# Kernel tuning notes

Hardware: AMD Instinct MI355X
Metric: run time of the kernel (lower is better)

The kernel has to match this reference:

```python
import jax, jax.numpy as jnp
from jax import lax
import numpy as np

B, CIN, COUT, WDIM, RES = 8, 512, 512, 512, 64


def setup_inputs() -> dict:
    key = jax.random.key(0)
    k0, k1, k2, k3 = jax.random.split(key, 4)
    x = jax.random.normal(k0, (B, CIN, RES, RES), dtype=jnp.float32)
    w = jax.random.normal(k1, (B, WDIM), dtype=jnp.float32)
    weight = jax.random.normal(k2, (COUT, CIN, 3, 3), dtype=jnp.float32)
    bias = jnp.zeros((COUT,), dtype=jnp.float32)
    affine_w = jax.random.normal(k3, (CIN, WDIM), dtype=jnp.float32) * 0.02
    affine_b = jnp.zeros((CIN,), dtype=jnp.float32)
    return {"x": x, "w": w, "weight": weight, "bias": bias,
            "affine_w": affine_w, "affine_b": affine_b}


def reference(x, w, weight, bias, affine_w, affine_b):
    # style: [B, Cin] = affine(w)
    style = w @ affine_w.T + affine_b
    b, cin, h, wd = x.shape
    cout = weight.shape[0]
    # per-sample modulated weight: [B, Cout, Cin, 3, 3]
    wmod = weight[None, :, :, :, :] * style[:, None, :, None, None]
    # grouped conv with groups = batch: lhs [1, B*Cin, H, W], rhs [B*Cout, Cin, 3, 3]
    lhs = x.reshape(1, b * cin, h, wd)
    rhs = wmod.reshape(b * cout, cin, 3, 3)
    y = lax.conv_general_dilated(
        lhs, rhs,
        window_strides=(1, 1),
        padding=[(1, 1), (1, 1)],
        dimension_numbers=("NCHW", "OIHW", "NCHW"),
        feature_group_count=b,
    )
    y = y.reshape(b, cout, h, wd)
    return y + bias[None, :, None, None]
```

## Files before the change

### kernel.cpp

```cpp
#include <hip/hip_runtime.h>
#include <cstdint>
#include <cstddef>

#define BATCH 8
#define CIN   512
#define COUT  512
#define RES   64
#define HW    4096
#define WDIM  512

typedef short bf16x8 __attribute__((ext_vector_type(8)));
typedef float f32x4  __attribute__((ext_vector_type(4)));
typedef unsigned short ushort8 __attribute__((ext_vector_type(8)));

typedef const __attribute__((address_space(1))) void* gas_ptr;
typedef __attribute__((address_space(3))) void*       las_ptr;

__device__ __forceinline__ unsigned short f2bf(float f) {
    unsigned int u = __float_as_uint(f);
    u += 0x7fffu + ((u >> 16) & 1u);
    return (unsigned short)(u >> 16);
}

__global__ __launch_bounds__(256) void prep_kernel(
    const float* __restrict__ w, const float* __restrict__ aw,
    const float* __restrict__ ab, float* __restrict__ style,
    unsigned short* __restrict__ zpage,
    const float* __restrict__ wt, unsigned short* __restrict__ wr)
{
    __shared__ float buf[4608];
    int bid = blockIdx.x;
    int t = threadIdx.x;
    if (bid < 1024) {
        if (bid == 0 && t < 128) zpage[t] = 0;
        int wv = t >> 6, lane = t & 63;
        int idx = bid * 4 + wv;
        int b = idx >> 9, ci = idx & 511;
        const float* wrow = w + b * WDIM;
        const float* arow = aw + (size_t)ci * WDIM;
        float s = 0.f;
#pragma unroll
        for (int i = 0; i < WDIM / 64; ++i) s += arow[lane + i * 64] * wrow[lane + i * 64];
#pragma unroll
        for (int off = 32; off; off >>= 1) s += __shfl_down(s, off);
        if (lane == 0) style[idx] = s + ab[ci];
    } else {
        int co = bid - 1024;
#pragma unroll
        for (int r = 0; r < 18; ++r) buf[r * 256 + t] = wt[(size_t)co * 4608 + r * 256 + t];
        __syncthreads();
#pragma unroll
        for (int r = 0; r < 18; ++r) {
            int idx = r * 256 + t;
            int tap = idx >> 9, ci = idx & 511;
            wr[(size_t)tap * (COUT * CIN) + co * CIN + ci] = f2bf(buf[ci * 9 + tap]);
        }
    }
}

__global__ __launch_bounds__(256) void modtrans_kernel(
    const float* __restrict__ x, const float* __restrict__ style,
    unsigned short* __restrict__ xs)
{
    __shared__ float tile[64][65];
    int t = threadIdx.x;
    int hw0 = blockIdx.x * 64, ci0 = blockIdx.y * 64, b = blockIdx.z;
    int sub = t >> 6, lane = t & 63;
#pragma unroll
    for (int r = 0; r < 16; ++r) {
        int ci = r * 4 + sub;
        float s = style[b * CIN + ci0 + ci];
        tile[ci][lane] = x[((size_t)(b * CIN + ci0 + ci)) * HW + hw0 + lane] * s;
    }
    __syncthreads();
    int ci8 = (t & 7) * 8;
#pragma unroll
    for (int r = 0; r < 2; ++r) {
        int hw = r * 32 + (t >> 3);
        ushort8 v;
#pragma unroll
        for (int j = 0; j < 8; ++j) v[j] = f2bf(tile[ci8 + j][hw]);
        *(ushort8*)&xs[((size_t)b * HW + hw0 + hw) * CIN + ci0 + ci8] = v;
    }
}

__global__ __launch_bounds__(256) void conv_kernel(
    const unsigned short* __restrict__ xs,
    const unsigned short* __restrict__ wr,
    const float* __restrict__ bias,
    const unsigned short* __restrict__ zpage,
    float* __restrict__ y)
{
    __shared__ __align__(16) unsigned short As[3 * 128 * 32];
    __shared__ __align__(16) unsigned short Bs[2 * 66 * 32];

    const int t   = threadIdx.x;
    const int bid = blockIdx.x;
    const int co0 = (bid >> 8) * 128;
    const int rem = bid & 255;
    const int h0  = (rem >> 3) * 2;
    const int b   = rem & 7;

    const int lane = t & 63;
    const int wv   = t >> 6;
    const int wm   = (wv & 1) * 64;
    const int wn   = (wv >> 1) * 64;
    const int r16  = lane & 15;
    const int quad = lane >> 4;

    if (t < 128) {
        int d = t >> 6, c = t & 63;
        int col = (c < 32) ? 0 : 65;
        Bs[(d * 66 + col) * 32 + (c & 31)] = 0;
    }

    f32x4 acc[4][4];
#pragma unroll
    for (int mi = 0; mi < 4; ++mi)
#pragma unroll
        for (int ni = 0; ni < 4; ++ni)
            acc[mi][ni] = (f32x4){0.f, 0.f, 0.f, 0.f};

    for (int kh = 0; kh < 3; ++kh) {
        const unsigned short* pA[6];
#pragma unroll
        for (int L = 0; L < 6; ++L) {
            int lin = L * 256 + t;
            int tap = kh * 3 + (lin >> 9);
            int q   = (lin >> 2) & 127;
            int c8  = ((lin & 3) ^ ((lin >> 3) & 3)) * 8;
            pA[L] = wr + (size_t)tap * (COUT * CIN) + (co0 + q) * CIN + c8;
        }
        const unsigned short* pB[2];
        int sB[2];
#pragma unroll
        for (int L = 0; L < 2; ++L) {
            int lin = L * 256 + t;
            int dh = lin >> 8, r8 = lin & 255;
            int wc = r8 >> 2;
            int rowp = dh * 66 + 1 + wc;
            int c8 = ((r8 & 3) ^ ((rowp >> 1) & 3)) * 8;
            int hp = h0 + dh + kh - 1;
            bool ok = (unsigned)hp < 64u;
            pB[L] = ok ? xs + ((size_t)b * HW + hp * 64 + wc) * CIN + c8 : zpage;
            sB[L] = ok ? 32 : 0;
        }

        for (int ch = 0; ch < 16; ++ch) {
#pragma unroll
            for (int L = 0; L < 6; ++L) {
                int lin = L * 256 + t;
                __builtin_amdgcn_global_load_lds((gas_ptr)pA[L], (las_ptr)&As[lin * 8], 16, 0, 0);
                pA[L] += 32;
            }
#pragma unroll
            for (int L = 0; L < 2; ++L) {
                int lin = L * 256 + t;
                int dh = lin >> 8, r8 = lin & 255;
                __builtin_amdgcn_global_load_lds((gas_ptr)pB[L],
                    (las_ptr)&Bs[(dh * 66 + 1) * 32 + r8 * 8], 16, 0, 0);
                pB[L] += sB[L];
            }
            __syncthreads();
#pragma unroll
            for (int kw = 0; kw < 3; ++kw) {
                bf16x8 af[4], bfv[4];
#pragma unroll
                for (int mi = 0; mi < 4; ++mi) {
                    int row = kw * 128 + wm + mi * 16 + r16;
                    int ck  = quad ^ ((row >> 1) & 3);
                    af[mi] = *(const bf16x8*)&As[row * 32 + ck * 8];
                }
#pragma unroll
                for (int ni = 0; ni < 4; ++ni) {
                    int n = wn + ni * 16 + r16;
                    int dh = n >> 6, wc = n & 63;
                    int row = dh * 66 + wc + kw;
                    int ck  = quad ^ ((row >> 1) & 3);
                    bfv[ni] = *(const bf16x8*)&Bs[row * 32 + ck * 8];
                }
#pragma unroll
                for (int mi = 0; mi < 4; ++mi)
#pragma unroll
                    for (int ni = 0; ni < 4; ++ni)
                        acc[mi][ni] = __builtin_amdgcn_mfma_f32_16x16x32_bf16(
                            af[mi], bfv[ni], acc[mi][ni], 0, 0, 0);
            }
            __syncthreads();
        }
    }

#pragma unroll
    for (int mi = 0; mi < 4; ++mi) {
#pragma unroll
        for (int r = 0; r < 4; ++r) {
            int m = co0 + wm + mi * 16 + quad * 4 + r;
            float bv = bias[m];
            size_t base = ((size_t)b * COUT + m) * HW + h0 * 64;
#pragma unroll
            for (int ni = 0; ni < 4; ++ni) {
                int n = wn + ni * 16 + r16;
                y[base + n] = acc[mi][ni][r] + bv;
            }
        }
    }
}

extern "C" void kernel_launch(void* const* d_in, const int* in_sizes, int n_in,
                              void* d_out, int out_size, void* d_ws, size_t ws_size,
                              hipStream_t stream)
{
    (void)in_sizes; (void)n_in; (void)out_size; (void)ws_size;
    const float* x    = (const float*)d_in[0];
    const float* w    = (const float*)d_in[1];
    const float* wt   = (const float*)d_in[2];
    const float* bias = (const float*)d_in[3];
    const float* aw   = (const float*)d_in[4];
    const float* ab   = (const float*)d_in[5];
    float* y = (float*)d_out;

    char* ws = (char*)d_ws;
    float*          style = (float*)ws;
    unsigned short* zpage = (unsigned short*)(ws + 16384);
    unsigned short* wr    = (unsigned short*)(ws + 32768);
    unsigned short* xs    = (unsigned short*)(ws + 4751360);

    prep_kernel<<<1536, 256, 0, stream>>>(w, aw, ab, style, zpage, wt, wr);
    modtrans_kernel<<<dim3(64, 8, 8), 256, 0, stream>>>(x, style, xs);
    conv_kernel<<<1024, 256, 0, stream>>>(xs, wr, bias, zpage, y);
}
```

Before: 268.7 us.

## Widen conv tile to four output rows with 512 threads and fuse prep kernels

The conv kernel now runs 8 waves per block and covers 4 output rows instead of 2. Each block's loaded weight tile is therefore reused across twice as many pixels, which halves the number of blocks and the total weight traffic. Separately, the style affine and the modulate/transpose step are folded into the prep kernel, so one launch and the global round trip of the style vector go away. The costs are a larger LDS footprint, 512-thread blocks that may lower occupancy, and fewer blocks (512) to spread across CUs.

Result: no change. 272.4 us (+1.4%).

```diff
diff --git a/kernel.cpp b/kernel.cpp
--- a/kernel.cpp
+++ b/kernel.cpp
@@ -11,6 +11,7 @@
 
 typedef short bf16x8 __attribute__((ext_vector_type(8)));
 typedef float f32x4  __attribute__((ext_vector_type(4)));
+typedef float f32x4v __attribute__((ext_vector_type(4)));
 typedef unsigned short ushort8 __attribute__((ext_vector_type(8)));
 
 typedef const __attribute__((address_space(1))) void* gas_ptr;
@@ -23,68 +24,80 @@
 }
 
 __global__ __launch_bounds__(256) void prep_kernel(
-    const float* __restrict__ w, const float* __restrict__ aw,
-    const float* __restrict__ ab, float* __restrict__ style,
-    unsigned short* __restrict__ zpage,
-    const float* __restrict__ wt, unsigned short* __restrict__ wr)
+    const float* __restrict__ x,  const float* __restrict__ w,
+    const float* __restrict__ aw, const float* __restrict__ ab,
+    const float* __restrict__ wt,
+    unsigned short* __restrict__ xs, unsigned short* __restrict__ wr,
+    unsigned short* __restrict__ zpage)
 {
-    __shared__ float buf[4608];
-    int bid = blockIdx.x;
-    int t = threadIdx.x;
-    if (bid < 1024) {
-        if (bid == 0 && t < 128) zpage[t] = 0;
-        int wv = t >> 6, lane = t & 63;
-        int idx = bid * 4 + wv;
-        int b = idx >> 9, ci = idx & 511;
-        const float* wrow = w + b * WDIM;
-        const float* arow = aw + (size_t)ci * WDIM;
-        float s = 0.f;
-#pragma unroll
-        for (int i = 0; i < WDIM / 64; ++i) s += arow[lane + i * 64] * wrow[lane + i * 64];
-#pragma unroll
-        for (int off = 32; off; off >>= 1) s += __shfl_down(s, off);
-        if (lane == 0) style[idx] = s + ab[ci];
+    __shared__ float sh[4608];
+    const int bid = blockIdx.x;
+    const int t   = threadIdx.x;
+
+    if (bid < 512) {
+        const int b   = bid & 7;
+        const int ci0 = ((bid >> 3) & 7) * 64;
+        const int hwb = (bid >> 6) * 512;
+
+        float* tile     = sh;
+        float* partials = sh + 4160;
+        float* styleS   = sh + 4416;
+
+        {
+            int cil = t >> 2, q = t & 3;
+            const f32x4v* arow = (const f32x4v*)(aw + (size_t)(ci0 + cil) * WDIM + q * 128);
+            const f32x4v* wrow = (const f32x4v*)(w + (size_t)b * WDIM + q * 128);
+            float s = 0.f;
+#pragma unroll
+            for (int i = 0; i < 32; ++i) {
+                f32x4v a = arow[i], ww = wrow[i];
+                s += a.x * ww.x + a.y * ww.y + a.z * ww.z + a.w * ww.w;
+            }
+            partials[t] = s;
+        }
+        __syncthreads();
+        if (t < 64)
+            styleS[t] = partials[t * 4] + partials[t * 4 + 1] + partials[t * 4 + 2]
+                      + partials[t * 4 + 3] + ab[ci0 + t];
+        __syncthreads();
+
+        int sub = t >> 6, lane = t & 63;
+        int ci8 = (t & 7) * 8;
+        for (int tl = 0; tl < 8; ++tl) {
+            int hw0 = hwb + tl * 64;
+#pragma unroll
+            for (int r = 0; r < 16; ++r) {
+                int ci = r * 4 + sub;
+                tile[ci * 65 + lane] =
+                    x[((size_t)(b * CIN + ci0 + ci)) * HW + hw0 + lane] * styleS[ci];
+            }
+            __syncthreads();
+#pragma unroll
+            for (int r = 0; r < 2; ++r) {
+                int hw = r * 32 + (t >> 3);
+                ushort8 v;
+#pragma unroll
+                for (int j = 0; j < 8; ++j) v[j] = f2bf(tile[(ci8 + j) * 65 + hw]);
+                *(ushort8*)&xs[((size_t)b * HW + hw0 + hw) * CIN + ci0 + ci8] = v;
+            }
+            __syncthreads();
+        }
     } else {
-        int co = bid - 1024;
-#pragma unroll
-        for (int r = 0; r < 18; ++r) buf[r * 256 + t] = wt[(size_t)co * 4608 + r * 256 + t];
+        if (bid == 512 && t < 128) zpage[t] = 0;
+        int co = bid - 512;
+#pragma unroll
+        for (int r = 0; r < 18; ++r) sh[r * 256 + t] = wt[(size_t)co * 4608 + r * 256 + t];
         __syncthreads();
 #pragma unroll
         for (int r = 0; r < 18; ++r) {
             int idx = r * 256 + t;
             int tap = idx >> 9, ci = idx & 511;
-            wr[(size_t)tap * (COUT * CIN) + co * CIN + ci] = f2bf(buf[ci * 9 + tap]);
-        }
-    }
-}
-
-__global__ __launch_bounds__(256) void modtrans_kernel(
-    const float* __restrict__ x, const float* __restrict__ style,
-    unsigned short* __restrict__ xs)
-{
-    __shared__ float tile[64][65];
-    int t = threadIdx.x;
-    int hw0 = blockIdx.x * 64, ci0 = blockIdx.y * 64, b = blockIdx.z;
-    int sub = t >> 6, lane = t & 63;
-#pragma unroll
-    for (int r = 0; r < 16; ++r) {
-        int ci = r * 4 + sub;
-        float s = style[b * CIN + ci0 + ci];
-        tile[ci][lane] = x[((size_t)(b * CIN + ci0 + ci)) * HW + hw0 + lane] * s;
-    }
-    __syncthreads();
-    int ci8 = (t & 7) * 8;
-#pragma unroll
-    for (int r = 0; r < 2; ++r) {
-        int hw = r * 32 + (t >> 3);
-        ushort8 v;
-#pragma unroll
-        for (int j = 0; j < 8; ++j) v[j] = f2bf(tile[ci8 + j][hw]);
-        *(ushort8*)&xs[((size_t)b * HW + hw0 + hw) * CIN + ci0 + ci8] = v;
-    }
-}
-
-__global__ __launch_bounds__(256) void conv_kernel(
+            wr[(size_t)tap * (COUT * CIN) + co * CIN + ci] = f2bf(sh[ci * 9 + tap]);
+        }
+    }
+}
+
+__global__ __launch_bounds__(512) void conv_kernel(
     const unsigned short* __restrict__ xs,
     const unsigned short* __restrict__ wr,
     const float* __restrict__ bias,
@@ -92,14 +105,13 @@
     float* __restrict__ y)
 {
     __shared__ __align__(16) unsigned short As[3 * 128 * 32];
-    __shared__ __align__(16) unsigned short Bs[2 * 66 * 32];
+    __shared__ __align__(16) unsigned short Bs[4 * 66 * 32];
 
     const int t   = threadIdx.x;
     const int bid = blockIdx.x;
-    const int co0 = (bid >> 8) * 128;
-    const int rem = bid & 255;
-    const int h0  = (rem >> 3) * 2;
-    const int b   = rem & 7;
+    const int b   = bid & 7;
+    const int h0  = ((bid >> 3) & 15) * 4;
+    const int co0 = (bid >> 7) * 128;
 
     const int lane = t & 63;
     const int wv   = t >> 6;
@@ -108,10 +120,10 @@
     const int r16  = lane & 15;
     const int quad = lane >> 4;
 
-    if (t < 128) {
-        int d = t >> 6, c = t & 63;
+    if (t < 256) {
+        int s = t >> 6, c = t & 63;
         int col = (c < 32) ? 0 : 65;
-        Bs[(d * 66 + col) * 32 + (c & 31)] = 0;
+        Bs[(s * 66 + col) * 32 + (c & 31)] = 0;
     }
 
     f32x4 acc[4][4];
@@ -122,10 +134,10 @@
             acc[mi][ni] = (f32x4){0.f, 0.f, 0.f, 0.f};
 
     for (int kh = 0; kh < 3; ++kh) {
-        const unsigned short* pA[6];
-#pragma unroll
-        for (int L = 0; L < 6; ++L) {
-            int lin = L * 256 + t;
+        const unsigned short* pA[3];
+#pragma unroll
+        for (int L = 0; L < 3; ++L) {
+            int lin = L * 512 + t;
             int tap = kh * 3 + (lin >> 9);
             int q   = (lin >> 2) & 127;
             int c8  = ((lin & 3) ^ ((lin >> 3) & 3)) * 8;
@@ -135,12 +147,12 @@
         int sB[2];
 #pragma unroll
         for (int L = 0; L < 2; ++L) {
-            int lin = L * 256 + t;
-            int dh = lin >> 8, r8 = lin & 255;
+            int lin = L * 512 + t;
+            int s  = lin >> 8, r8 = lin & 255;
             int wc = r8 >> 2;
-            int rowp = dh * 66 + 1 + wc;
+            int rowp = s * 66 + 1 + wc;
             int c8 = ((r8 & 3) ^ ((rowp >> 1) & 3)) * 8;
-            int hp = h0 + dh + kh - 1;
+            int hp = h0 + kh - 1 + s;
             bool ok = (unsigned)hp < 64u;
             pB[L] = ok ? xs + ((size_t)b * HW + hp * 64 + wc) * CIN + c8 : zpage;
             sB[L] = ok ? 32 : 0;
@@ -148,17 +160,17 @@
 
         for (int ch = 0; ch < 16; ++ch) {
 #pragma unroll
-            for (int L = 0; L < 6; ++L) {
-                int lin = L * 256 + t;
+            for (int L = 0; L < 3; ++L) {
+                int lin = L * 512 + t;
                 __builtin_amdgcn_global_load_lds((gas_ptr)pA[L], (las_ptr)&As[lin * 8], 16, 0, 0);
                 pA[L] += 32;
             }
 #pragma unroll
             for (int L = 0; L < 2; ++L) {
-                int lin = L * 256 + t;
-                int dh = lin >> 8, r8 = lin & 255;
+                int lin = L * 512 + t;
+                int s = lin >> 8, r8 = lin & 255;
                 __builtin_amdgcn_global_load_lds((gas_ptr)pB[L],
-                    (las_ptr)&Bs[(dh * 66 + 1) * 32 + r8 * 8], 16, 0, 0);
+                    (las_ptr)&Bs[(s * 66 + 1) * 32 + r8 * 8], 16, 0, 0);
                 pB[L] += sB[L];
             }
             __syncthreads();
@@ -220,12 +232,10 @@
     float* y = (float*)d_out;
 
     char* ws = (char*)d_ws;
-    float*          style = (float*)ws;
     unsigned short* zpage = (unsigned short*)(ws + 16384);
     unsigned short* wr    = (unsigned short*)(ws + 32768);
     unsigned short* xs    = (unsigned short*)(ws + 4751360);
 
-    prep_kernel<<<1536, 256, 0, stream>>>(w, aw, ab, style, zpage, wt, wr);
-    modtrans_kernel<<<dim3(64, 8, 8), 256, 0, stream>>>(x, style, xs);
-    conv_kernel<<<1024, 256, 0, stream>>>(xs, wr, bias, zpage, y);
-}
+    prep_kernel<<<1024, 256, 0, stream>>>(x, w, aw, ab, wt, xs, wr, zpage);
+    conv_kernel<<<512, 512, 0, stream>>>(xs, wr, bias, zpage, y);
+}
```
